# Kernel tuning notes

Measured on AMD Instinct MI355X. Metric: run time of the kernel, lower is better.

Reference implementation:

```python
import jax, jax.numpy as jnp
import numpy as np

H = 1024
NH = 16
DK = H // NH
FF = 4 * H
EPS = 1e-5

def layer_norm(x, g, b):
    mu = jnp.mean(x, axis=-1, keepdims=True)
    var = jnp.mean(jnp.square(x - mu), axis=-1, keepdims=True)
    return (x - mu) * jax.lax.rsqrt(var + EPS) * g + b

def setup_inputs() -> dict:
    key = jax.random.key(0)
    ks = jax.random.split(key, 12)
    s = 0.02
    return {
        "x": jax.random.normal(ks[0], (2, 2048, H), dtype=jnp.float32),
        "ln_g": jnp.ones((H,), jnp.float32),
        "ln_b": jnp.zeros((H,), jnp.float32),
        "wq": jax.random.normal(ks[1], (H, H), jnp.float32) * s,
        "bq": jnp.zeros((H,), jnp.float32),
        "wk": jax.random.normal(ks[2], (H, H), jnp.float32) * s,
        "bk": jnp.zeros((H,), jnp.float32),
        "wv": jax.random.normal(ks[3], (H, H), jnp.float32) * s,
        "bv": jnp.zeros((H,), jnp.float32),
        "w1": jax.random.normal(ks[4], (H, FF), jnp.float32) * s,
        "b1": jnp.zeros((FF,), jnp.float32),
        "w2": jax.random.normal(ks[5], (FF, H), jnp.float32) * s,
        "b2": jnp.zeros((H,), jnp.float32),
    }

def reference(x, ln_g, ln_b, wq, bq, wk, bk, wv, bv, w1, b1, w2, b2):
    B, S, _ = x.shape
    # Note: the torch module reuses the SAME LayerNorm params for both norms.
    h = layer_norm(x, ln_g, ln_b)
    q = (h @ wq + bq).reshape(B, S, NH, DK).transpose(0, 2, 1, 3)  # [B,NH,S,DK]
    k = (h @ wk + bk).reshape(B, S, NH, DK).transpose(0, 2, 1, 3)
    v = (h @ wv + bv).reshape(B, S, NH, DK).transpose(0, 2, 1, 3)
    scores = jnp.einsum('bhqd,bhkd->bhqk', q, k) / jnp.sqrt(jnp.float32(DK))
    att = jax.nn.softmax(scores, axis=-1)  # [B,NH,S,S]
    att_out = jnp.einsum('bhqk,bhkd->bhqd', att, v)
    att_out = att_out.transpose(0, 2, 1, 3).reshape(B, S, H)
    x = x + att_out  # dropout_prob=0 -> identity
    h2 = layer_norm(x, ln_g, ln_b)
    mlp = jax.nn.gelu(h2 @ w1 + b1, approximate=False) @ w2 + b2
    x = x + mlp
    return (x, att)
```

## Files before the change

### kernel.cpp

```cpp
#include <hip/hip_runtime.h>
#include <hip/hip_bf16.h>

typedef unsigned short u16;
typedef __attribute__((ext_vector_type(8))) short short8;
typedef __attribute__((ext_vector_type(4))) float f32x4;
typedef __attribute__((ext_vector_type(4))) unsigned int u32x4;

__device__ inline u16 f2bf(float f) {
    unsigned int u = __float_as_uint(f);
    unsigned int r = (u + 0x7fffu + ((u >> 16) & 1u)) >> 16;
    return (u16)r;
}

__device__ __forceinline__ void gload16(const u16* g, u16* l) {
    __builtin_amdgcn_global_load_lds(
        (const __attribute__((address_space(1))) void*)g,
        (__attribute__((address_space(3))) void*)l, 16, 0, 0);
}

__global__ void transpose_cvt(const float* __restrict__ in, u16* __restrict__ out,
                              int K, int N) {
    __shared__ float tile[32][33];
    int n0 = blockIdx.x * 32, k0 = blockIdx.y * 32;
    int tx = threadIdx.x, ty = threadIdx.y;
#pragma unroll
    for (int i = 0; i < 4; i++)
        tile[ty + i * 8][tx] = in[(size_t)(k0 + ty + i * 8) * N + n0 + tx];
    __syncthreads();
#pragma unroll
    for (int i = 0; i < 4; i++)
        out[(size_t)(n0 + ty + i * 8) * K + k0 + tx] = f2bf(tile[tx][ty + i * 8]);
}

template <bool ADD>
__global__ void ln_kernel(const float* __restrict__ x, const float* __restrict__ add,
                          const float* __restrict__ g, const float* __restrict__ b,
                          float* __restrict__ xa_out, u16* __restrict__ h_out) {
    int row = blockIdx.x;
    int t = threadIdx.x;
    float4 v = ((const float4*)(x + (size_t)row * 1024))[t];
    if (ADD) {
        float4 a = ((const float4*)(add + (size_t)row * 1024))[t];
        v.x += a.x; v.y += a.y; v.z += a.z; v.w += a.w;
        ((float4*)(xa_out + (size_t)row * 1024))[t] = v;
    }
    float s = v.x + v.y + v.z + v.w;
    float sq = v.x * v.x + v.y * v.y + v.z * v.z + v.w * v.w;
#pragma unroll
    for (int off = 32; off >= 1; off >>= 1) {
        s  += __shfl_xor(s, off);
        sq += __shfl_xor(sq, off);
    }
    __shared__ float ps[4], pq[4];
    int wid = t >> 6, lane = t & 63;
    if (lane == 0) { ps[wid] = s; pq[wid] = sq; }
    __syncthreads();
    s  = ps[0] + ps[1] + ps[2] + ps[3];
    sq = pq[0] + pq[1] + pq[2] + pq[3];
    float mu  = s * (1.0f / 1024.0f);
    float var = sq * (1.0f / 1024.0f) - mu * mu;
    float rstd = rsqrtf(var + 1e-5f);
    float4 gv = ((const float4*)g)[t];
    float4 bv = ((const float4*)b)[t];
    ushort4 o;
    o.x = f2bf((v.x - mu) * rstd * gv.x + bv.x);
    o.y = f2bf((v.y - mu) * rstd * gv.y + bv.y);
    o.z = f2bf((v.z - mu) * rstd * gv.z + bv.z);
    o.w = f2bf((v.w - mu) * rstd * gv.w + bv.w);
    ((ushort4*)(h_out + (size_t)row * 1024))[t] = o;
}

__device__ __forceinline__ void xcd_swizzle(int BN, int& m0, int& n0) {
    int gx = gridDim.x;
    int lin = blockIdx.x + gx * blockIdx.y;
    int cpx = (gx * gridDim.y) >> 3;
    int swz = (lin & 7) * cpx + (lin >> 3);
    n0 = (swz % gx) * BN;
    m0 = (swz / gx) * 128;
}

template <int BN>
__device__ __forceinline__ void gemm_core(
    const u16* __restrict__ A, const u16* __restrict__ Bt, int K,
    int m0, int n0, u16* As, u16* Bs, f32x4 (*acc)[BN / 32]) {
    const int NB = BN / 32;
    int t = threadIdx.x, lane = t & 63, w = t >> 6;
    int l15 = lane & 15, lhi = lane >> 4;
    int wm = (w >> 1) * 64, wn = (w & 1) * (BN / 2);

    int srow8 = (lane >> 3) & 7;
    int scol = ((lane & 7) ^ srow8) * 8;
    const u16* Ag = A + (size_t)(m0 + w * 32 + (lane >> 3)) * K + scol;
    const u16* Bg = Bt + (size_t)(n0 + w * (BN / 4) + (lane >> 3)) * K + scol;
    u16* AsW = As + (w * 32) * 64;
    u16* BsW = Bs + (w * (BN / 4)) * 64;

    int rs = (l15 & 7) << 3;

    for (int k0 = 0; k0 < K; k0 += 64) {
        __syncthreads();
#pragma unroll
        for (int j = 0; j < 4; j++)
            gload16(Ag + k0 + (size_t)j * 8 * K, AsW + j * 8 * 64);
#pragma unroll
        for (int j = 0; j < NB; j++)
            gload16(Bg + k0 + (size_t)j * 8 * K, BsW + j * 8 * 64);
        __syncthreads();
#pragma unroll
        for (int ks = 0; ks < 2; ks++) {
            short8 af[4], bfr[NB];
#pragma unroll
            for (int mi = 0; mi < 4; mi++)
                af[mi] = *(const short8*)&As[(wm + mi * 16 + l15) * 64 +
                                             ((ks * 32 + lhi * 8) ^ rs)];
#pragma unroll
            for (int ni = 0; ni < NB; ni++)
                bfr[ni] = *(const short8*)&Bs[(wn + ni * 16 + l15) * 64 +
                                              ((ks * 32 + lhi * 8) ^ rs)];
#pragma unroll
            for (int mi = 0; mi < 4; mi++)
#pragma unroll
                for (int ni = 0; ni < NB; ni++)
                    acc[mi][ni] = __builtin_amdgcn_mfma_f32_16x16x32_bf16(
                        af[mi], bfr[ni], acc[mi][ni], 0, 0, 0);
        }
    }
}

__global__ __launch_bounds__(256) void qkv_gemm(
    const u16* __restrict__ A,
    const u16* __restrict__ wqT, const u16* __restrict__ wkT, const u16* __restrict__ wvT,
    const float* __restrict__ bq, const float* __restrict__ bk, const float* __restrict__ bv,
    u16* __restrict__ qb, u16* __restrict__ kb, u16* __restrict__ vtb) {
    __shared__ alignas(16) u16 As[128 * 64];
    __shared__ alignas(16) u16 Bs[128 * 64];
    int z = blockIdx.z;
    const u16* Bt = z == 0 ? wqT : (z == 1 ? wkT : wvT);
    const float* bias = z == 0 ? bq : (z == 1 ? bk : bv);
    float scale = z == 0 ? 0.18033688011112042f : 1.0f;
    int m0, n0;
    xcd_swizzle(128, m0, n0);

    f32x4 acc[4][4] = {};
    gemm_core<128>(A, Bt, 1024, m0, n0, As, Bs, acc);

    int t = threadIdx.x, lane = t & 63, w = t >> 6;
    int l15 = lane & 15, lhi = lane >> 4;
    int wm = (w >> 1) * 64, wn = (w & 1) * 64;
#pragma unroll
    for (int mi = 0; mi < 4; mi++)
#pragma unroll
        for (int ni = 0; ni < 4; ni++)
#pragma unroll
            for (int r = 0; r < 4; r++) {
                int row = m0 + wm + mi * 16 + lhi * 4 + r;
                int col = n0 + wn + ni * 16 + l15;
                u16 o = f2bf((acc[mi][ni][r] + bias[col]) * scale);
                int bb = row >> 11, ss = row & 2047, hh = col >> 6, dd = col & 63;
                if (z < 2) {
                    u16* outp = z == 0 ? qb : kb;
                    outp[(((size_t)(bb * 16 + hh) * 2048) + ss) * 64 + dd] = o;
                } else {
                    vtb[(((size_t)(bb * 16 + hh) * 64) + dd) * 2048 + ss] = o;
                }
            }
}

template <int MODE, int BN>
__global__ __launch_bounds__(256) void mlp_gemm(
    const u16* __restrict__ A, const u16* __restrict__ Bt,
    const float* __restrict__ bias, void* __restrict__ outp,
    const float* __restrict__ resid, int N, int K) {
    __shared__ alignas(16) u16 As[128 * 64];
    __shared__ alignas(16) u16 Bs[BN * 64];
    int m0, n0;
    xcd_swizzle(BN, m0, n0);

    f32x4 acc[4][BN / 32] = {};
    gemm_core<BN>(A, Bt, K, m0, n0, As, Bs, acc);

    int t = threadIdx.x, lane = t & 63, w = t >> 6;
    int l15 = lane & 15, lhi = lane >> 4;
    int wm = (w >> 1) * 64, wn = (w & 1) * (BN / 2);
#pragma unroll
    for (int mi = 0; mi < 4; mi++)
#pragma unroll
        for (int ni = 0; ni < BN / 32; ni++)
#pragma unroll
            for (int r = 0; r < 4; r++) {
                int row = m0 + wm + mi * 16 + lhi * 4 + r;
                int col = n0 + wn + ni * 16 + l15;
                float val = acc[mi][ni][r] + bias[col];
                if (MODE == 2) {
                    float gl = 0.5f * val * (1.0f + erff(val * 0.70710678118654752f));
                    ((u16*)outp)[(size_t)row * N + col] = f2bf(gl);
                } else {
                    ((float*)outp)[(size_t)row * N + col] =
                        val + resid[(size_t)row * N + col];
                }
            }
}

__global__ __launch_bounds__(512) void attn_kernel(
    const u16* __restrict__ q, const u16* __restrict__ k,
    const u16* __restrict__ vt, float* __restrict__ att,
    float* __restrict__ attout) {
    const int S = 2048;
    int bx = blockIdx.x;
    int swz = (bx & 7) * 64 + (bx >> 3);
    int bh = swz >> 4;
    int qb = swz & 15;
    int t = threadIdx.x, w = t >> 6, lane = t & 63;
    int l15 = lane & 15, lhi = lane >> 4;
    int q0 = qb * 128 + w * 16;

    const u16* qh = q + (size_t)bh * S * 64;
    const u16* kh = k + (size_t)bh * S * 64;
    const u16* vh = vt + (size_t)bh * 64 * S;

    __shared__ alignas(16) u16 Ks[2][64][64];
    __shared__ alignas(16) u16 Vs[2][64][64];

    int srow = lane >> 3;
    int scol = (((lane & 7) ^ srow)) * 8;
    const u16* kg = kh + (size_t)(w * 8 + srow) * 64 + scol;
    const u16* vg = vh + (size_t)(w * 8 + srow) * 2048 + scol;
    u16* ksl[2] = {&Ks[0][w * 8][0], &Ks[1][w * 8][0]};
    u16* vsl[2] = {&Vs[0][w * 8][0], &Vs[1][w * 8][0]};

    short8 aq0 = *(const short8*)&qh[(size_t)(q0 + l15) * 64 + lhi * 8];
    short8 aq1 = *(const short8*)&qh[(size_t)(q0 + l15) * 64 + 32 + lhi * 8];

    f32x4 z = {0.f, 0.f, 0.f, 0.f};
    float sum = 0.f;

    gload16(kg, ksl[0]);
    for (int i = 0; i < 32; i++) {
        __syncthreads();
        if (i + 1 < 32) gload16(kg + (size_t)(i + 1) * 64 * 64, ksl[(i + 1) & 1]);
        const u16(*Kb)[64] = Ks[i & 1];
#pragma unroll
        for (int sub = 0; sub < 4; sub++) {
            int R = sub * 16 + l15;
            int cs = (R & 7) << 3;
            short8 b0 = *(const short8*)&Kb[R][(lhi * 8) ^ cs];
            short8 b1 = *(const short8*)&Kb[R][(32 + lhi * 8) ^ cs];
            f32x4 s = z;
            s = __builtin_amdgcn_mfma_f32_16x16x32_bf16(b0, aq0, s, 0, 0, 0);
            s = __builtin_amdgcn_mfma_f32_16x16x32_bf16(b1, aq1, s, 0, 0, 0);
            sum += __builtin_exp2f(s[0]) + __builtin_exp2f(s[1]) +
                   __builtin_exp2f(s[2]) + __builtin_exp2f(s[3]);
        }
    }
    sum += __shfl_xor(sum, 16);
    sum += __shfl_xor(sum, 32);
    float lrl = -__log2f(sum);

    f32x4 o[4];
#pragma unroll
    for (int ni = 0; ni < 4; ni++) o[ni] = z;

    float* attq = att + ((size_t)bh * S + q0) * S;

    gload16(kg, ksl[0]);
    gload16(vg, vsl[0]);
    for (int i = 0; i < 32; i++) {
        __syncthreads();
        if (i + 1 < 32) {
            gload16(kg + (size_t)(i + 1) * 64 * 64, ksl[(i + 1) & 1]);
            gload16(vg + (i + 1) * 64, vsl[(i + 1) & 1]);
        }
        const u16(*Kb)[64] = Ks[i & 1];
        const u16(*Vb)[64] = Vs[i & 1];
#pragma unroll
        for (int kp2 = 0; kp2 < 2; kp2++) {
            int ktb = i * 64 + kp2 * 32;
            unsigned int v0, v1, v2, v3;
#pragma unroll
            for (int half = 0; half < 2; half++) {
                int R = kp2 * 32 + half * 16 + l15;
                int cs = (R & 7) << 3;
                short8 kb0 = *(const short8*)&Kb[R][(lhi * 8) ^ cs];
                short8 kb1 = *(const short8*)&Kb[R][(32 + lhi * 8) ^ cs];
                f32x4 s = {lrl, lrl, lrl, lrl};
                s = __builtin_amdgcn_mfma_f32_16x16x32_bf16(kb0, aq0, s, 0, 0, 0);
                s = __builtin_amdgcn_mfma_f32_16x16x32_bf16(kb1, aq1, s, 0, 0, 0);
                f32x4 p;
#pragma unroll
                for (int r = 0; r < 4; r++) p[r] = __builtin_exp2f(s[r]);
                *(f32x4*)&attq[(size_t)l15 * S + ktb + half * 16 + lhi * 4] = p;
                unsigned int lo = (unsigned int)f2bf(p[0]) |
                                  ((unsigned int)f2bf(p[1]) << 16);
                unsigned int hi = (unsigned int)f2bf(p[2]) |
                                  ((unsigned int)f2bf(p[3]) << 16);
                if (half == 0) { v0 = lo; v1 = hi; } else { v2 = lo; v3 = hi; }
            }
            int srcA = l15 + (((lhi * 2) & 3) << 4);
            int srcB = srcA + 16;
            unsigned int a0 = (unsigned int)__shfl((int)v0, srcA);
            unsigned int a1 = (unsigned int)__shfl((int)v1, srcA);
            unsigned int bb0 = (unsigned int)__shfl((int)v0, srcB);
            unsigned int bb1 = (unsigned int)__shfl((int)v1, srcB);
            unsigned int c0 = (unsigned int)__shfl((int)v2, srcA);
            unsigned int c1 = (unsigned int)__shfl((int)v3, srcA);
            unsigned int d0 = (unsigned int)__shfl((int)v2, srcB);
            unsigned int d1 = (unsigned int)__shfl((int)v3, srcB);
            bool hw = lhi >= 2;
            u32x4 wv;
            wv[0] = hw ? c0 : a0;
            wv[1] = hw ? c1 : a1;
            wv[2] = hw ? d0 : bb0;
            wv[3] = hw ? d1 : bb1;
            short8 pa = __builtin_bit_cast(short8, wv);
#pragma unroll
            for (int ni = 0; ni < 4; ni++) {
                int R = ni * 16 + l15;
                int cs = (R & 7) << 3;
                short8 vb = *(const short8*)&Vb[R][(kp2 * 32 + lhi * 8) ^ cs];
                o[ni] = __builtin_amdgcn_mfma_f32_16x16x32_bf16(pa, vb, o[ni], 0, 0, 0);
            }
        }
    }

    int bb = bh >> 4, hh = bh & 15;
#pragma unroll
    for (int ni = 0; ni < 4; ni++)
#pragma unroll
        for (int r = 0; r < 4; r++) {
            int srw = q0 + lhi * 4 + r;
            attout[((size_t)(bb * 2048 + srw)) * 1024 + hh * 64 + ni * 16 + l15] = o[ni][r];
        }
}

extern "C" void kernel_launch(void* const* d_in, const int* in_sizes, int n_in,
                              void* d_out, int out_size, void* d_ws, size_t ws_size,
                              hipStream_t stream) {
    const float* x    = (const float*)d_in[0];
    const float* ln_g = (const float*)d_in[1];
    const float* ln_b = (const float*)d_in[2];
    const float* wq   = (const float*)d_in[3];
    const float* bq   = (const float*)d_in[4];
    const float* wk   = (const float*)d_in[5];
    const float* bk   = (const float*)d_in[6];
    const float* wv   = (const float*)d_in[7];
    const float* bv   = (const float*)d_in[8];
    const float* w1   = (const float*)d_in[9];
    const float* b1   = (const float*)d_in[10];
    const float* w2   = (const float*)d_in[11];
    const float* b2   = (const float*)d_in[12];

    char* ws = (char*)d_ws;
    const size_t MB = 1024 * 1024;
    u16* wqT = (u16*)(ws + 0 * MB);
    u16* wkT = (u16*)(ws + 2 * MB);
    u16* wvT = (u16*)(ws + 4 * MB);
    u16* w1T = (u16*)(ws + 6 * MB);
    u16* w2T = (u16*)(ws + 14 * MB);
    u16* h1  = (u16*)(ws + 22 * MB);
    u16* qb  = (u16*)(ws + 30 * MB);
    u16* kb  = (u16*)(ws + 38 * MB);
    u16* vtb = (u16*)(ws + 46 * MB);
    u16* ub  = (u16*)(ws + 22 * MB);
    float* attout = (float*)(ws + 54 * MB);
    float* xa = (float*)(ws + 70 * MB);
    u16* h2  = (u16*)(ws + 86 * MB);

    float* xout = (float*)d_out;
    float* att  = xout + (size_t)2 * 2048 * 1024;

    dim3 tb(32, 8);
    transpose_cvt<<<dim3(32, 32), tb, 0, stream>>>(wq, wqT, 1024, 1024);
    transpose_cvt<<<dim3(32, 32), tb, 0, stream>>>(wk, wkT, 1024, 1024);
    transpose_cvt<<<dim3(32, 32), tb, 0, stream>>>(wv, wvT, 1024, 1024);
    transpose_cvt<<<dim3(128, 32), tb, 0, stream>>>(w1, w1T, 1024, 4096);
    transpose_cvt<<<dim3(32, 128), tb, 0, stream>>>(w2, w2T, 4096, 1024);

    ln_kernel<false><<<4096, 256, 0, stream>>>(x, nullptr, ln_g, ln_b, nullptr, h1);

    qkv_gemm<<<dim3(8, 32, 3), 256, 0, stream>>>(h1, wqT, wkT, wvT, bq, bk, bv,
                                                 qb, kb, vtb);

    attn_kernel<<<512, 512, 0, stream>>>(qb, kb, vtb, att, attout);

    ln_kernel<true><<<4096, 256, 0, stream>>>(x, attout, ln_g, ln_b, xa, h2);

    mlp_gemm<2, 128><<<dim3(32, 32), 256, 0, stream>>>(h2, w1T, b1, ub, nullptr, 4096, 1024);
    mlp_gemm<3, 64><<<dim3(16, 32), 256, 0, stream>>>(ub, w2T, b2, xout, xa, 1024, 4096);
}
```

Measured before the change: 428.9 us.

## Drop LDS staging in attention kernel, load K/V straight from global

Removes the double-buffered shared-memory staging of K and V tiles and the per-tile block barriers in the attention kernel. Each wave now reads its K and V fragments directly from global memory (relying on L1/L2 for reuse). Blocks shrink from 512 to 256 threads with 64 query rows each, and twice as many blocks are launched. This avoids LDS traffic and synchronisation, but it gives up explicit sharing of K/V across waves and may issue more uncoalesced global loads.

```diff
diff --git a/kernel.cpp b/kernel.cpp
--- a/kernel.cpp
+++ b/kernel.cpp
@@ -201,56 +201,39 @@
             }
 }
 
-__global__ __launch_bounds__(512) void attn_kernel(
+__global__ __launch_bounds__(256) void attn_kernel(
     const u16* __restrict__ q, const u16* __restrict__ k,
     const u16* __restrict__ vt, float* __restrict__ att,
     float* __restrict__ attout) {
     const int S = 2048;
     int bx = blockIdx.x;
-    int swz = (bx & 7) * 64 + (bx >> 3);
-    int bh = swz >> 4;
-    int qb = swz & 15;
+    int swz = (bx & 7) * 128 + (bx >> 3);
+    int bh = swz >> 5;
+    int qb = swz & 31;
     int t = threadIdx.x, w = t >> 6, lane = t & 63;
     int l15 = lane & 15, lhi = lane >> 4;
-    int q0 = qb * 128 + w * 16;
+    int q0 = qb * 64 + w * 16;
 
     const u16* qh = q + (size_t)bh * S * 64;
     const u16* kh = k + (size_t)bh * S * 64;
     const u16* vh = vt + (size_t)bh * 64 * S;
 
-    __shared__ alignas(16) u16 Ks[2][64][64];
-    __shared__ alignas(16) u16 Vs[2][64][64];
-
-    int srow = lane >> 3;
-    int scol = (((lane & 7) ^ srow)) * 8;
-    const u16* kg = kh + (size_t)(w * 8 + srow) * 64 + scol;
-    const u16* vg = vh + (size_t)(w * 8 + srow) * 2048 + scol;
-    u16* ksl[2] = {&Ks[0][w * 8][0], &Ks[1][w * 8][0]};
-    u16* vsl[2] = {&Vs[0][w * 8][0], &Vs[1][w * 8][0]};
-
     short8 aq0 = *(const short8*)&qh[(size_t)(q0 + l15) * 64 + lhi * 8];
     short8 aq1 = *(const short8*)&qh[(size_t)(q0 + l15) * 64 + 32 + lhi * 8];
 
     f32x4 z = {0.f, 0.f, 0.f, 0.f};
     float sum = 0.f;
 
-    gload16(kg, ksl[0]);
-    for (int i = 0; i < 32; i++) {
-        __syncthreads();
-        if (i + 1 < 32) gload16(kg + (size_t)(i + 1) * 64 * 64, ksl[(i + 1) & 1]);
-        const u16(*Kb)[64] = Ks[i & 1];
-#pragma unroll
-        for (int sub = 0; sub < 4; sub++) {
-            int R = sub * 16 + l15;
-            int cs = (R & 7) << 3;
-            short8 b0 = *(const short8*)&Kb[R][(lhi * 8) ^ cs];
-            short8 b1 = *(const short8*)&Kb[R][(32 + lhi * 8) ^ cs];
-            f32x4 s = z;
-            s = __builtin_amdgcn_mfma_f32_16x16x32_bf16(b0, aq0, s, 0, 0, 0);
-            s = __builtin_amdgcn_mfma_f32_16x16x32_bf16(b1, aq1, s, 0, 0, 0);
-            sum += __builtin_exp2f(s[0]) + __builtin_exp2f(s[1]) +
-                   __builtin_exp2f(s[2]) + __builtin_exp2f(s[3]);
-        }
+#pragma unroll 4
+    for (int kt = 0; kt < 128; kt++) {
+        const u16* kr = &kh[(size_t)(kt * 16 + l15) * 64 + lhi * 8];
+        short8 b0 = *(const short8*)kr;
+        short8 b1 = *(const short8*)(kr + 32);
+        f32x4 s = z;
+        s = __builtin_amdgcn_mfma_f32_16x16x32_bf16(b0, aq0, s, 0, 0, 0);
+        s = __builtin_amdgcn_mfma_f32_16x16x32_bf16(b1, aq1, s, 0, 0, 0);
+        sum += __builtin_exp2f(s[0]) + __builtin_exp2f(s[1]) +
+               __builtin_exp2f(s[2]) + __builtin_exp2f(s[3]);
     }
     sum += __shfl_xor(sum, 16);
     sum += __shfl_xor(sum, 32);
@@ -262,63 +245,50 @@
 
     float* attq = att + ((size_t)bh * S + q0) * S;
 
-    gload16(kg, ksl[0]);
-    gload16(vg, vsl[0]);
-    for (int i = 0; i < 32; i++) {
-        __syncthreads();
-        if (i + 1 < 32) {
-            gload16(kg + (size_t)(i + 1) * 64 * 64, ksl[(i + 1) & 1]);
-            gload16(vg + (i + 1) * 64, vsl[(i + 1) & 1]);
+#pragma unroll 2
+    for (int g = 0; g < 64; g++) {
+        int ktb = g * 32;
+        unsigned int v0, v1, v2, v3;
+#pragma unroll
+        for (int half = 0; half < 2; half++) {
+            const u16* kr = &kh[(size_t)(ktb + half * 16 + l15) * 64 + lhi * 8];
+            short8 kb0 = *(const short8*)kr;
+            short8 kb1 = *(const short8*)(kr + 32);
+            f32x4 s = {lrl, lrl, lrl, lrl};
+            s = __builtin_amdgcn_mfma_f32_16x16x32_bf16(kb0, aq0, s, 0, 0, 0);
+            s = __builtin_amdgcn_mfma_f32_16x16x32_bf16(kb1, aq1, s, 0, 0, 0);
+            f32x4 p;
+#pragma unroll
+            for (int r = 0; r < 4; r++) p[r] = __builtin_exp2f(s[r]);
+            *(f32x4*)&attq[(size_t)l15 * S + ktb + half * 16 + lhi * 4] = p;
+            unsigned int lo = (unsigned int)f2bf(p[0]) |
+                              ((unsigned int)f2bf(p[1]) << 16);
+            unsigned int hi = (unsigned int)f2bf(p[2]) |
+                              ((unsigned int)f2bf(p[3]) << 16);
+            if (half == 0) { v0 = lo; v1 = hi; } else { v2 = lo; v3 = hi; }
         }
-        const u16(*Kb)[64] = Ks[i & 1];
-        const u16(*Vb)[64] = Vs[i & 1];
-#pragma unroll
-        for (int kp2 = 0; kp2 < 2; kp2++) {
-            int ktb = i * 64 + kp2 * 32;
-            unsigned int v0, v1, v2, v3;
-#pragma unroll
-            for (int half = 0; half < 2; half++) {
-                int R = kp2 * 32 + half * 16 + l15;
-                int cs = (R & 7) << 3;
-                short8 kb0 = *(const short8*)&Kb[R][(lhi * 8) ^ cs];
-                short8 kb1 = *(const short8*)&Kb[R][(32 + lhi * 8) ^ cs];
-                f32x4 s = {lrl, lrl, lrl, lrl};
-                s = __builtin_amdgcn_mfma_f32_16x16x32_bf16(kb0, aq0, s, 0, 0, 0);
-                s = __builtin_amdgcn_mfma_f32_16x16x32_bf16(kb1, aq1, s, 0, 0, 0);
-                f32x4 p;
-#pragma unroll
-                for (int r = 0; r < 4; r++) p[r] = __builtin_exp2f(s[r]);
-                *(f32x4*)&attq[(size_t)l15 * S + ktb + half * 16 + lhi * 4] = p;
-                unsigned int lo = (unsigned int)f2bf(p[0]) |
-                                  ((unsigned int)f2bf(p[1]) << 16);
-                unsigned int hi = (unsigned int)f2bf(p[2]) |
-                                  ((unsigned int)f2bf(p[3]) << 16);
-                if (half == 0) { v0 = lo; v1 = hi; } else { v2 = lo; v3 = hi; }
-            }
-            int srcA = l15 + (((lhi * 2) & 3) << 4);
-            int srcB = srcA + 16;
-            unsigned int a0 = (unsigned int)__shfl((int)v0, srcA);
-            unsigned int a1 = (unsigned int)__shfl((int)v1, srcA);
-            unsigned int bb0 = (unsigned int)__shfl((int)v0, srcB);
-            unsigned int bb1 = (unsigned int)__shfl((int)v1, srcB);
-            unsigned int c0 = (unsigned int)__shfl((int)v2, srcA);
-            unsigned int c1 = (unsigned int)__shfl((int)v3, srcA);
-            unsigned int d0 = (unsigned int)__shfl((int)v2, srcB);
-            unsigned int d1 = (unsigned int)__shfl((int)v3, srcB);
-            bool hw = lhi >= 2;
-            u32x4 wv;
-            wv[0] = hw ? c0 : a0;
-            wv[1] = hw ? c1 : a1;
-            wv[2] = hw ? d0 : bb0;
-            wv[3] = hw ? d1 : bb1;
-            short8 pa = __builtin_bit_cast(short8, wv);
-#pragma unroll
-            for (int ni = 0; ni < 4; ni++) {
-                int R = ni * 16 + l15;
-                int cs = (R & 7) << 3;
-                short8 vb = *(const short8*)&Vb[R][(kp2 * 32 + lhi * 8) ^ cs];
-                o[ni] = __builtin_amdgcn_mfma_f32_16x16x32_bf16(pa, vb, o[ni], 0, 0, 0);
-            }
+        int srcA = l15 + (((lhi * 2) & 3) << 4);
+        int srcB = srcA + 16;
+        unsigned int a0 = (unsigned int)__shfl((int)v0, srcA);
+        unsigned int a1 = (unsigned int)__shfl((int)v1, srcA);
+        unsigned int bb0 = (unsigned int)__shfl((int)v0, srcB);
+        unsigned int bb1 = (unsigned int)__shfl((int)v1, srcB);
+        unsigned int c0 = (unsigned int)__shfl((int)v2, srcA);
+        unsigned int c1 = (unsigned int)__shfl((int)v3, srcA);
+        unsigned int d0 = (unsigned int)__shfl((int)v2, srcB);
+        unsigned int d1 = (unsigned int)__shfl((int)v3, srcB);
+        bool hw = lhi >= 2;
+        u32x4 wv;
+        wv[0] = hw ? c0 : a0;
+        wv[1] = hw ? c1 : a1;
+        wv[2] = hw ? d0 : bb0;
+        wv[3] = hw ? d1 : bb1;
+        short8 pa = __builtin_bit_cast(short8, wv);
+#pragma unroll
+        for (int ni = 0; ni < 4; ni++) {
+            short8 vb = *(const short8*)&vh[(size_t)(ni * 16 + l15) * 2048 +
+                                            ktb + lhi * 8];
+            o[ni] = __builtin_amdgcn_mfma_f32_16x16x32_bf16(pa, vb, o[ni], 0, 0, 0);
         }
     }
 
@@ -380,7 +350,7 @@
     qkv_gemm<<<dim3(8, 32, 3), 256, 0, stream>>>(h1, wqT, wkT, wvT, bq, bk, bv,
                                                  qb, kb, vtb);
 
-    attn_kernel<<<512, 512, 0, stream>>>(qb, kb, vtb, att, attout);
+    attn_kernel<<<1024, 256, 0, stream>>>(qb, kb, vtb, att, attout);
 
     ln_kernel<true><<<4096, 256, 0, stream>>>(x, attout, ln_g, ln_b, xa, h2);
 
```

Result: slower. 621.6 us (+44.9%).

## Triple-buffer attention K/V tiles with explicit vmcnt waits; drop GEMM XCD swizzle

Applied to the files above, without the earlier changes.

The attention kernel moves from double to triple buffering of K and V tiles in LDS, prefetching two tiles ahead. Plain __syncthreads is replaced by explicit s_waitcnt vmcnt counts and s_barrier calls wrapped in scheduling barriers, so global loads overlap more compute. Separately, the GEMM kernels drop the XCD-aware block swizzle and use direct blockIdx tiling, which may change L2 locality. The extra LDS buffer raises shared memory use per block, and the hand-tuned wait counts depend on exact load ordering.

```diff
diff --git a/kernel.cpp b/kernel.cpp
--- a/kernel.cpp
+++ b/kernel.cpp
@@ -70,15 +70,6 @@
     ((ushort4*)(h_out + (size_t)row * 1024))[t] = o;
 }
 
-__device__ __forceinline__ void xcd_swizzle(int BN, int& m0, int& n0) {
-    int gx = gridDim.x;
-    int lin = blockIdx.x + gx * blockIdx.y;
-    int cpx = (gx * gridDim.y) >> 3;
-    int swz = (lin & 7) * cpx + (lin >> 3);
-    n0 = (swz % gx) * BN;
-    m0 = (swz / gx) * 128;
-}
-
 template <int BN>
 __device__ __forceinline__ void gemm_core(
     const u16* __restrict__ A, const u16* __restrict__ Bt, int K,
@@ -138,8 +129,7 @@
     const u16* Bt = z == 0 ? wqT : (z == 1 ? wkT : wvT);
     const float* bias = z == 0 ? bq : (z == 1 ? bk : bv);
     float scale = z == 0 ? 0.18033688011112042f : 1.0f;
-    int m0, n0;
-    xcd_swizzle(128, m0, n0);
+    int n0 = blockIdx.x * 128, m0 = blockIdx.y * 128;
 
     f32x4 acc[4][4] = {};
     gemm_core<128>(A, Bt, 1024, m0, n0, As, Bs, acc);
@@ -173,8 +163,7 @@
     const float* __restrict__ resid, int N, int K) {
     __shared__ alignas(16) u16 As[128 * 64];
     __shared__ alignas(16) u16 Bs[BN * 64];
-    int m0, n0;
-    xcd_swizzle(BN, m0, n0);
+    int n0 = blockIdx.x * BN, m0 = blockIdx.y * 128;
 
     f32x4 acc[4][BN / 32] = {};
     gemm_core<BN>(A, Bt, K, m0, n0, As, Bs, acc);
@@ -218,15 +207,13 @@
     const u16* kh = k + (size_t)bh * S * 64;
     const u16* vh = vt + (size_t)bh * 64 * S;
 
-    __shared__ alignas(16) u16 Ks[2][64][64];
-    __shared__ alignas(16) u16 Vs[2][64][64];
+    __shared__ alignas(16) u16 Ks[3][64][64];
+    __shared__ alignas(16) u16 Vs[3][64][64];
 
     int srow = lane >> 3;
     int scol = (((lane & 7) ^ srow)) * 8;
     const u16* kg = kh + (size_t)(w * 8 + srow) * 64 + scol;
     const u16* vg = vh + (size_t)(w * 8 + srow) * 2048 + scol;
-    u16* ksl[2] = {&Ks[0][w * 8][0], &Ks[1][w * 8][0]};
-    u16* vsl[2] = {&Vs[0][w * 8][0], &Vs[1][w * 8][0]};
 
     short8 aq0 = *(const short8*)&qh[(size_t)(q0 + l15) * 64 + lhi * 8];
     short8 aq1 = *(const short8*)&qh[(size_t)(q0 + l15) * 64 + 32 + lhi * 8];
@@ -234,11 +221,15 @@
     f32x4 z = {0.f, 0.f, 0.f, 0.f};
     float sum = 0.f;
 
-    gload16(kg, ksl[0]);
+    gload16(kg, &Ks[0][w * 8][0]);
+    gload16(kg + 4096, &Ks[1][w * 8][0]);
     for (int i = 0; i < 32; i++) {
-        __syncthreads();
-        if (i + 1 < 32) gload16(kg + (size_t)(i + 1) * 64 * 64, ksl[(i + 1) & 1]);
-        const u16(*Kb)[64] = Ks[i & 1];
+        if (i < 31) asm volatile("s_waitcnt vmcnt(1)" ::: "memory");
+        else        asm volatile("s_waitcnt vmcnt(0)" ::: "memory");
+        __builtin_amdgcn_sched_barrier(0);
+        __builtin_amdgcn_s_barrier();
+        __builtin_amdgcn_sched_barrier(0);
+        const u16(*Kb)[64] = Ks[i % 3];
 #pragma unroll
         for (int sub = 0; sub < 4; sub++) {
             int R = sub * 16 + l15;
@@ -251,6 +242,11 @@
             sum += __builtin_exp2f(s[0]) + __builtin_exp2f(s[1]) +
                    __builtin_exp2f(s[2]) + __builtin_exp2f(s[3]);
         }
+        __builtin_amdgcn_sched_barrier(0);
+        __builtin_amdgcn_s_barrier();
+        __builtin_amdgcn_sched_barrier(0);
+        if (i + 2 < 32)
+            gload16(kg + (size_t)(i + 2) * 4096, &Ks[(i + 2) % 3][w * 8][0]);
     }
     sum += __shfl_xor(sum, 16);
     sum += __shfl_xor(sum, 32);
@@ -262,16 +258,20 @@
 
     float* attq = att + ((size_t)bh * S + q0) * S;
 
-    gload16(kg, ksl[0]);
-    gload16(vg, vsl[0]);
+    __syncthreads();
+
+    gload16(kg, &Ks[0][w * 8][0]);
+    gload16(vg, &Vs[0][w * 8][0]);
+    gload16(kg + 4096, &Ks[1][w * 8][0]);
+    gload16(vg + 64, &Vs[1][w * 8][0]);
     for (int i = 0; i < 32; i++) {
-        __syncthreads();
-        if (i + 1 < 32) {
-            gload16(kg + (size_t)(i + 1) * 64 * 64, ksl[(i + 1) & 1]);
-            gload16(vg + (i + 1) * 64, vsl[(i + 1) & 1]);
-        }
-        const u16(*Kb)[64] = Ks[i & 1];
-        const u16(*Vb)[64] = Vs[i & 1];
+        if (i < 31) asm volatile("s_waitcnt vmcnt(2)" ::: "memory");
+        else        asm volatile("s_waitcnt vmcnt(0)" ::: "memory");
+        __builtin_amdgcn_sched_barrier(0);
+        __builtin_amdgcn_s_barrier();
+        __builtin_amdgcn_sched_barrier(0);
+        const u16(*Kb)[64] = Ks[i % 3];
+        const u16(*Vb)[64] = Vs[i % 3];
 #pragma unroll
         for (int kp2 = 0; kp2 < 2; kp2++) {
             int ktb = i * 64 + kp2 * 32;
@@ -320,6 +320,13 @@
                 o[ni] = __builtin_amdgcn_mfma_f32_16x16x32_bf16(pa, vb, o[ni], 0, 0, 0);
             }
         }
+        __builtin_amdgcn_sched_barrier(0);
+        __builtin_amdgcn_s_barrier();
+        __builtin_amdgcn_sched_barrier(0);
+        if (i + 2 < 32) {
+            gload16(kg + (size_t)(i + 2) * 4096, &Ks[(i + 2) % 3][w * 8][0]);
+            gload16(vg + (i + 2) * 64, &Vs[(i + 2) % 3][w * 8][0]);
+        }
     }
 
     int bb = bh >> 4, hh = bh & 15;
```

After: 445.5 us. +3.9%, slower.

## Halve attention block size, use explicit waitcnt barriers, drop GEMM XCD swizzle

Applied to the files above, without the earlier changes.

The attention kernel now runs 1024 blocks of 256 threads, each covering 64 queries instead of 128, and every wave loads two 8-row slices of the K/V tiles. The __syncthreads calls are replaced by explicit s_waitcnt vmcnt plus s_barrier with sched_barriers, so in the second pass the next tile's loads can stay in flight. The GEMM kernels drop the XCD swizzle and use plain blockIdx tiling. The goal is better occupancy and latency hiding in attention, but the K/V tile traffic per query doubles and GEMM L2 locality across XCDs may get worse.

```diff
diff --git a/kernel.cpp b/kernel.cpp
--- a/kernel.cpp
+++ b/kernel.cpp
@@ -70,15 +70,6 @@
     ((ushort4*)(h_out + (size_t)row * 1024))[t] = o;
 }
 
-__device__ __forceinline__ void xcd_swizzle(int BN, int& m0, int& n0) {
-    int gx = gridDim.x;
-    int lin = blockIdx.x + gx * blockIdx.y;
-    int cpx = (gx * gridDim.y) >> 3;
-    int swz = (lin & 7) * cpx + (lin >> 3);
-    n0 = (swz % gx) * BN;
-    m0 = (swz / gx) * 128;
-}
-
 template <int BN>
 __device__ __forceinline__ void gemm_core(
     const u16* __restrict__ A, const u16* __restrict__ Bt, int K,
@@ -138,8 +129,7 @@
     const u16* Bt = z == 0 ? wqT : (z == 1 ? wkT : wvT);
     const float* bias = z == 0 ? bq : (z == 1 ? bk : bv);
     float scale = z == 0 ? 0.18033688011112042f : 1.0f;
-    int m0, n0;
-    xcd_swizzle(128, m0, n0);
+    int n0 = blockIdx.x * 128, m0 = blockIdx.y * 128;
 
     f32x4 acc[4][4] = {};
     gemm_core<128>(A, Bt, 1024, m0, n0, As, Bs, acc);
@@ -173,8 +163,7 @@
     const float* __restrict__ resid, int N, int K) {
     __shared__ alignas(16) u16 As[128 * 64];
     __shared__ alignas(16) u16 Bs[BN * 64];
-    int m0, n0;
-    xcd_swizzle(BN, m0, n0);
+    int n0 = blockIdx.x * BN, m0 = blockIdx.y * 128;
 
     f32x4 acc[4][BN / 32] = {};
     gemm_core<BN>(A, Bt, K, m0, n0, As, Bs, acc);
@@ -201,18 +190,18 @@
             }
 }
 
-__global__ __launch_bounds__(512) void attn_kernel(
+__global__ __launch_bounds__(256) void attn_kernel(
     const u16* __restrict__ q, const u16* __restrict__ k,
     const u16* __restrict__ vt, float* __restrict__ att,
     float* __restrict__ attout) {
     const int S = 2048;
     int bx = blockIdx.x;
-    int swz = (bx & 7) * 64 + (bx >> 3);
-    int bh = swz >> 4;
-    int qb = swz & 15;
+    int swz = (bx & 7) * 128 + (bx >> 3);
+    int bh = swz >> 5;
+    int qb = swz & 31;
     int t = threadIdx.x, w = t >> 6, lane = t & 63;
     int l15 = lane & 15, lhi = lane >> 4;
-    int q0 = qb * 128 + w * 16;
+    int q0 = qb * 64 + w * 16;
 
     const u16* qh = q + (size_t)bh * S * 64;
     const u16* kh = k + (size_t)bh * S * 64;
@@ -223,10 +212,10 @@
 
     int srow = lane >> 3;
     int scol = (((lane & 7) ^ srow)) * 8;
-    const u16* kg = kh + (size_t)(w * 8 + srow) * 64 + scol;
-    const u16* vg = vh + (size_t)(w * 8 + srow) * 2048 + scol;
-    u16* ksl[2] = {&Ks[0][w * 8][0], &Ks[1][w * 8][0]};
-    u16* vsl[2] = {&Vs[0][w * 8][0], &Vs[1][w * 8][0]};
+    const u16* kg0 = kh + (size_t)(w * 16 + srow) * 64 + scol;
+    const u16* kg1 = kh + (size_t)(w * 16 + 8 + srow) * 64 + scol;
+    const u16* vg0 = vh + (size_t)(w * 16 + srow) * 2048 + scol;
+    const u16* vg1 = vh + (size_t)(w * 16 + 8 + srow) * 2048 + scol;
 
     short8 aq0 = *(const short8*)&qh[(size_t)(q0 + l15) * 64 + lhi * 8];
     short8 aq1 = *(const short8*)&qh[(size_t)(q0 + l15) * 64 + 32 + lhi * 8];
@@ -234,10 +223,17 @@
     f32x4 z = {0.f, 0.f, 0.f, 0.f};
     float sum = 0.f;
 
-    gload16(kg, ksl[0]);
+    gload16(kg0, &Ks[0][w * 16][0]);
+    gload16(kg1, &Ks[0][w * 16 + 8][0]);
     for (int i = 0; i < 32; i++) {
-        __syncthreads();
-        if (i + 1 < 32) gload16(kg + (size_t)(i + 1) * 64 * 64, ksl[(i + 1) & 1]);
+        asm volatile("s_waitcnt vmcnt(0)" ::: "memory");
+        __builtin_amdgcn_sched_barrier(0);
+        __builtin_amdgcn_s_barrier();
+        __builtin_amdgcn_sched_barrier(0);
+        if (i + 1 < 32) {
+            gload16(kg0 + (size_t)(i + 1) * 4096, &Ks[(i + 1) & 1][w * 16][0]);
+            gload16(kg1 + (size_t)(i + 1) * 4096, &Ks[(i + 1) & 1][w * 16 + 8][0]);
+        }
         const u16(*Kb)[64] = Ks[i & 1];
 #pragma unroll
         for (int sub = 0; sub < 4; sub++) {
@@ -262,13 +258,23 @@
 
     float* attq = att + ((size_t)bh * S + q0) * S;
 
-    gload16(kg, ksl[0]);
-    gload16(vg, vsl[0]);
+    __syncthreads();
+
+    gload16(kg0, &Ks[0][w * 16][0]);
+    gload16(kg1, &Ks[0][w * 16 + 8][0]);
+    gload16(vg0, &Vs[0][w * 16][0]);
+    gload16(vg1, &Vs[0][w * 16 + 8][0]);
     for (int i = 0; i < 32; i++) {
-        __syncthreads();
+        if (i == 0) asm volatile("s_waitcnt vmcnt(0)" ::: "memory");
+        else        asm volatile("s_waitcnt vmcnt(8)" ::: "memory");
+        __builtin_amdgcn_sched_barrier(0);
+        __builtin_amdgcn_s_barrier();
+        __builtin_amdgcn_sched_barrier(0);
         if (i + 1 < 32) {
-            gload16(kg + (size_t)(i + 1) * 64 * 64, ksl[(i + 1) & 1]);
-            gload16(vg + (i + 1) * 64, vsl[(i + 1) & 1]);
+            gload16(kg0 + (size_t)(i + 1) * 4096, &Ks[(i + 1) & 1][w * 16][0]);
+            gload16(kg1 + (size_t)(i + 1) * 4096, &Ks[(i + 1) & 1][w * 16 + 8][0]);
+            gload16(vg0 + (i + 1) * 64, &Vs[(i + 1) & 1][w * 16][0]);
+            gload16(vg1 + (i + 1) * 64, &Vs[(i + 1) & 1][w * 16 + 8][0]);
         }
         const u16(*Kb)[64] = Ks[i & 1];
         const u16(*Vb)[64] = Vs[i & 1];
@@ -380,7 +386,7 @@
     qkv_gemm<<<dim3(8, 32, 3), 256, 0, stream>>>(h1, wqT, wkT, wvT, bq, bk, bv,
                                                  qb, kb, vtb);
 
-    attn_kernel<<<512, 512, 0, stream>>>(qb, kb, vtb, att, attout);
+    attn_kernel<<<1024, 256, 0, stream>>>(qb, kb, vtb, att, attout);
 
     ln_kernel<true><<<4096, 256, 0, stream>>>(x, attout, ln_g, ln_b, xa, h2);
 
```

New measurement: 444.8 us. 3.7% more time.
